# Kernel tuning notes

Measured on AMD Instinct MI355X. Metric: run time of the kernel, lower is better.

## Reference

```python
import jax, jax.numpy as jnp
import numpy as np

NUM_HEADS = 8


def _attn(q, k, v, scale):
    # q: [B,H,Nq,d], k/v: [B,H,Nk,d]
    a = jax.nn.softmax(jnp.einsum('bhqd,bhkd->bhqk', q, k) * scale, axis=-1)
    return jnp.einsum('bhqk,bhkd->bhqd', a, v)


def setup_inputs() -> dict:
    key = jax.random.key(0)
    k1, k2, k3 = jax.random.split(key, 3)
    B, N, C = 8, 1024, 768
    x = jax.random.normal(k1, (B, N, C), dtype=jnp.float32)
    w_qkv = jax.random.normal(k2, (3 * C, C), dtype=jnp.float32) * 0.02
    w_proj = jax.random.normal(k3, (C, C), dtype=jnp.float32) * 0.02
    b_proj = jnp.zeros((C,), dtype=jnp.float32)
    return {"x": x, "w_qkv": w_qkv, "w_proj": w_proj, "b_proj": b_proj}


def reference(x, w_qkv, w_proj, b_proj):
    B, N, C = x.shape
    H = NUM_HEADS
    hd = C // H            # full head dim (scale uses this, per the source)
    g = hd // 3            # per-group head dim
    scale = hd ** (-0.5)

    qkv = (x @ w_qkv.T).reshape(B, N, 3, H, hd).transpose(2, 0, 3, 1, 4)  # [3,B,H,N,hd]
    q, k, v = qkv[0], qkv[1], qkv[2]

    q3, q4, q5 = q[..., :g], q[..., g:2 * g], q[..., 2 * g:]
    k3, k4, k5 = k[..., :g], k[..., g:2 * g], k[..., 2 * g:]
    v3, v4, v5 = v[..., :g], v[..., g:2 * g], v[..., 2 * g:]

    def merge(o):  # [B,H,N,g] -> [B,N,H*g]
        return o.transpose(0, 2, 1, 3).reshape(B, N, C // 3)

    x3 = merge(_attn(q4, jnp.concatenate([k3, k4], axis=2), jnp.concatenate([v3, v4], axis=2), scale))
    x4 = merge(_attn(q5, jnp.concatenate([k3, k5], axis=2), jnp.concatenate([v3, v5], axis=2), scale))
    x5 = merge(_attn(q5, jnp.concatenate([k4, k5], axis=2), jnp.concatenate([v4, v5], axis=2), scale))

    out = jnp.concatenate([x3, x4, x5], axis=2)
    return out @ w_proj.T + b_proj
```

## Files before the change

kernel.cpp:

```cpp
#include <hip/hip_runtime.h>
#include <hip/hip_bf16.h>

typedef unsigned short u16;
typedef __attribute__((ext_vector_type(8))) short short8;
typedef __attribute__((ext_vector_type(4))) float f32x4;
typedef __attribute__((ext_vector_type(4))) unsigned uint32x4;

__device__ __forceinline__ u16 f2b(float f) {
  unsigned u = __builtin_bit_cast(unsigned, f);
  unsigned r = u + 0x7fffu + ((u >> 16) & 1u);
  return (u16)(r >> 16);
}

__device__ __forceinline__ unsigned pkbf16(float lo, float hi) {
  unsigned r;
  asm("v_cvt_pk_bf16_f32 %0, %1, %2" : "=v"(r) : "v"(lo), "v"(hi));
  return r;
}

#define GLD_LDS16(gp, lp) __builtin_amdgcn_global_load_lds( \
    (const __attribute__((address_space(1))) void*)(gp),    \
    (__attribute__((address_space(3))) void*)(lp), 16, 0, 0)

__global__ __launch_bounds__(256) void cvt3(
    const float* __restrict__ x, const float* __restrict__ wq, const float* __restrict__ wp,
    u16* __restrict__ xb, u16* __restrict__ wqb, u16* __restrict__ wpb)
{
  const int NX = 8192 * 768 / 4, NQ = 2304 * 768 / 4, NP = 768 * 768 / 4;
  int i = blockIdx.x * 256 + threadIdx.x;
  if (i < NX) {
    float4 v = *(const float4*)&x[(size_t)i * 4];
    uint2 pk; pk.x = pkbf16(v.x, v.y); pk.y = pkbf16(v.z, v.w);
    *(uint2*)&xb[(size_t)i * 4] = pk;
  } else if (i < NX + NQ) {
    int j = i - NX;
    float sc = (j < 147456) ? 0.14724447f : 1.0f;
    float4 v = *(const float4*)&wq[(size_t)j * 4];
    uint2 pk; pk.x = pkbf16(v.x * sc, v.y * sc); pk.y = pkbf16(v.z * sc, v.w * sc);
    *(uint2*)&wqb[(size_t)j * 4] = pk;
  } else if (i < NX + NQ + NP) {
    int j = i - NX - NQ;
    int oo = (j * 4) / 768, ii = (j * 4) % 768;
    int a = ii >> 8, h = (ii >> 5) & 7, c = ii & 31;
    float4 v = *(const float4*)&wp[(size_t)j * 4];
    uint2 pk; pk.x = pkbf16(v.x, v.y); pk.y = pkbf16(v.z, v.w);
    *(uint2*)&wpb[oo * 768 + h * 96 + a * 32 + c] = pk;
  }
}

__global__ __launch_bounds__(256) void gemm_bt(
    const u16* __restrict__ A, const u16* __restrict__ Bt,
    u16* __restrict__ Cb, float* __restrict__ Cf, const float* __restrict__ bias,
    u16* __restrict__ vt_out, int M, int N, int K)
{
  __shared__ u16 Al[128 * 32];
  __shared__ u16 Bl[128 * 32];
  const int tid = threadIdx.x;
  const int lane = tid & 63, wave = tid >> 6;
  const int wr = wave >> 1, wc = wave & 1;
  const int g = lane >> 4, c16 = lane & 15;
  const int m0 = blockIdx.y * 128, n0 = blockIdx.x * 128;

  f32x4 acc[4][4] = {};

  const int c0 = tid, c1 = tid + 256;
  const int r0 = c0 >> 2, o0 = (c0 & 3) * 8;
  const int r1 = c1 >> 2, o1 = (c1 & 3) * 8;
  const u16* a0 = A + (size_t)(m0 + r0) * K + o0;
  const u16* a1 = A + (size_t)(m0 + r1) * K + o1;
  const u16* b0 = Bt + (size_t)(n0 + r0) * K + o0;
  const u16* b1 = Bt + (size_t)(n0 + r1) * K + o1;

  for (int k0 = 0; k0 < K; k0 += 32) {
    GLD_LDS16(a0 + k0, Al + c0 * 8);
    GLD_LDS16(a1 + k0, Al + c1 * 8);
    GLD_LDS16(b0 + k0, Bl + c0 * 8);
    GLD_LDS16(b1 + k0, Bl + c1 * 8);
    __syncthreads();
    short8 af[4], bfr[4];
#pragma unroll
    for (int m = 0; m < 4; ++m)
      af[m] = *(const short8*)&Al[(wr * 64 + m * 16 + c16) * 32 + g * 8];
#pragma unroll
    for (int n = 0; n < 4; ++n)
      bfr[n] = *(const short8*)&Bl[(wc * 64 + n * 16 + c16) * 32 + g * 8];
#pragma unroll
    for (int m = 0; m < 4; ++m)
#pragma unroll
      for (int n = 0; n < 4; ++n)
        acc[m][n] = __builtin_amdgcn_mfma_f32_16x16x32_bf16(af[m], bfr[n], acc[m][n], 0, 0, 0);
    __syncthreads();
  }

  if (Cb) {
    if (vt_out && n0 >= 1536) {
#pragma unroll
      for (int m = 0; m < 4; ++m) {
        const int row0 = m0 + wr * 64 + m * 16 + g * 4;
        const int bb = row0 >> 10, nb = row0 & 1023;
        const int chunk = nb & ~31, o = nb & 31;
        const int slot0 = ((o >> 2) & 3) * 8 + ((o >> 4) & 1) * 4;
#pragma unroll
        for (int n = 0; n < 4; ++n) {
          const int colg = n0 - 1536 + wc * 64 + n * 16 + c16;
          const int hh = colg / 96, dd = colg % 96;
          uint2 pk;
          pk.x = pkbf16(acc[m][n][0], acc[m][n][1]);
          pk.y = pkbf16(acc[m][n][2], acc[m][n][3]);
          *(uint2*)&vt_out[((size_t)(bb * 8 + hh) * 96 + dd) * 1024 + chunk + slot0] = pk;
        }
      }
    } else {
#pragma unroll
      for (int m = 0; m < 4; ++m) {
        const int row = m0 + wr * 64 + m * 16 + g * 4;
#pragma unroll
        for (int n = 0; n < 4; ++n) {
          const int col = n0 + wc * 64 + n * 16 + c16;
#pragma unroll
          for (int j = 0; j < 4; ++j)
            Cb[(size_t)(row + j) * N + col] = f2b(acc[m][n][j]);
        }
      }
    }
  } else {
#pragma unroll
    for (int m = 0; m < 4; ++m) {
      const int row = m0 + wr * 64 + m * 16 + g * 4;
#pragma unroll
      for (int n = 0; n < 4; ++n) {
        const int col = n0 + wc * 64 + n * 16 + c16;
        const float bb = bias[col];
#pragma unroll
        for (int j = 0; j < 4; ++j)
          Cf[(size_t)(row + j) * N + col] = acc[m][n][j] + bb;
      }
    }
  }
}

__global__ __attribute__((amdgpu_flat_work_group_size(256, 256)))
__attribute__((amdgpu_waves_per_eu(2, 4)))
void attn_kernel(
    const u16* __restrict__ qkv, const u16* __restrict__ vt, u16* __restrict__ feat)
{
  __shared__ u16 smem[2 * 2560 + 64 * 72];
  u16* Kl = smem;
  u16* Vl = smem + 2 * 2560;

  const int tid = threadIdx.x;
  const int lane = tid & 63, wave = tid >> 6;
  const int g = lane >> 4, c16 = lane & 15;
  const int id = blockIdx.x;
  const int h = id & 7;
  const int r3 = id >> 3;
  const int aidx = r3 % 3;
  const int t2 = r3 / 3;
  const int qt = t2 & 7, b = t2 >> 3;
  const int bh = b * 8 + h;
  const int q0 = qt * 128 + wave * 32;
  const size_t tb = (size_t)b * 1024;

  const int p0 = (aidx == 2) ? 1 : 0;
  const int p1 = (aidx == 0) ? 1 : 2;
  const int qoff = (aidx == 0) ? 32 : 64;

  short8 qf[2];
#pragma unroll
  for (int m = 0; m < 2; ++m)
    qf[m] = *(const short8*)&qkv[(tb + q0 + m * 16 + c16) * 2304 + h * 96 + qoff + 8 * g];

  short8 ones;
#pragma unroll
  for (int i = 0; i < 8; ++i) ones[i] = (short)0x3F80;

  f32x4 acc[2][2] = {};
  f32x4 lsv[2] = {};

  const int kkey = tid >> 2, kcc = tid & 3;
  const int vd = tid >> 3, vc = tid & 7;
  const int P[2] = { p0, p1 };
  uint4 kst[2], vst[2];
#pragma unroll
  for (int i = 0; i < 2; ++i) {
    kst[i] = *(const uint4*)&qkv[(tb + kkey) * 2304 + 768 + h * 96 + P[i] * 32 + kcc * 8];
    vst[i] = *(const uint4*)&vt[((size_t)bh * 96 + P[i] * 32 + vd) * 1024 + vc * 8];
  }

  for (int t = 0; t < 16; ++t) {
    __syncthreads();
#pragma unroll
    for (int i = 0; i < 2; ++i) {
      *(uint4*)&Kl[i * 2560 + kkey * 40 + kcc * 8] = kst[i];
      *(uint4*)&Vl[(i * 32 + vd) * 72 + vc * 8] = vst[i];
    }
    if (t < 15) {
      int kv0 = (t + 1) * 64;
#pragma unroll
      for (int i = 0; i < 2; ++i) {
        kst[i] = *(const uint4*)&qkv[(tb + kv0 + kkey) * 2304 + 768 + h * 96 + P[i] * 32 + kcc * 8];
        vst[i] = *(const uint4*)&vt[((size_t)bh * 96 + P[i] * 32 + vd) * 1024 + kv0 + vc * 8];
      }
    }
    __syncthreads();

#pragma unroll
    for (int u = 0; u < 2; ++u) {
      short8 kf[4], vf[2][2];
#pragma unroll
      for (int n = 0; n < 4; ++n)
        kf[n] = *(const short8*)&Kl[u * 2560 + (n * 16 + c16) * 40 + g * 8];
#pragma unroll
      for (int n = 0; n < 2; ++n)
#pragma unroll
        for (int kk = 0; kk < 2; ++kk)
          vf[n][kk] = *(const short8*)&Vl[(u * 32 + n * 16 + c16) * 72 + kk * 32 + g * 8];

      const f32x4 z = {0.f, 0.f, 0.f, 0.f};
#pragma unroll
      for (int m = 0; m < 2; ++m) {
        f32x4 St[4];
        __builtin_amdgcn_s_setprio(1);
#pragma unroll
        for (int n = 0; n < 4; ++n)
          St[n] = __builtin_amdgcn_mfma_f32_16x16x32_bf16(kf[n], qf[m], z, 0, 0, 0);
        __builtin_amdgcn_s_setprio(0);
        short8 pa[2];
#pragma unroll
        for (int kk = 0; kk < 2; ++kk) {
          uint32x4 w;
          w.x = pkbf16(__builtin_amdgcn_exp2f(St[2 * kk][0]),     __builtin_amdgcn_exp2f(St[2 * kk][1]));
          w.y = pkbf16(__builtin_amdgcn_exp2f(St[2 * kk][2]),     __builtin_amdgcn_exp2f(St[2 * kk][3]));
          w.z = pkbf16(__builtin_amdgcn_exp2f(St[2 * kk + 1][0]), __builtin_amdgcn_exp2f(St[2 * kk + 1][1]));
          w.w = pkbf16(__builtin_amdgcn_exp2f(St[2 * kk + 1][2]), __builtin_amdgcn_exp2f(St[2 * kk + 1][3]));
          pa[kk] = __builtin_bit_cast(short8, w);
        }
        __builtin_amdgcn_s_setprio(1);
#pragma unroll
        for (int n = 0; n < 2; ++n)
#pragma unroll
          for (int kk = 0; kk < 2; ++kk)
            acc[m][n] = __builtin_amdgcn_mfma_f32_16x16x32_bf16(pa[kk], vf[n][kk], acc[m][n], 0, 0, 0);
#pragma unroll
        for (int kk = 0; kk < 2; ++kk)
          lsv[m] = __builtin_amdgcn_mfma_f32_16x16x32_bf16(pa[kk], ones, lsv[m], 0, 0, 0);
        __builtin_amdgcn_s_setprio(0);
      }
    }
  }

  __syncthreads();
  u16* Ol = smem + wave * 1024;
#pragma unroll
  for (int m = 0; m < 2; ++m) {
    f32x4 inv;
#pragma unroll
    for (int r = 0; r < 4; ++r) inv[r] = 1.0f / lsv[m][r];
#pragma unroll
    for (int n = 0; n < 2; ++n)
#pragma unroll
      for (int r = 0; r < 4; ++r)
        Ol[(m * 16 + g * 4 + r) * 32 + n * 16 + c16] = f2b(acc[m][n][r] * inv[r]);
  }
#pragma unroll
  for (int i = 0; i < 2; ++i) {
    int idx = lane + 64 * i;
    int row = idx >> 2, q4 = idx & 3;
    uint4 val = *(const uint4*)&Ol[row * 32 + q4 * 8];
    *(uint4*)&feat[(tb + q0 + row) * 768 + h * 96 + aidx * 32 + q4 * 8] = val;
  }
}

extern "C" void kernel_launch(void* const* d_in, const int* in_sizes, int n_in,
                              void* d_out, int out_size, void* d_ws, size_t ws_size,
                              hipStream_t stream) {
  const float* x  = (const float*)d_in[0];
  const float* wq = (const float*)d_in[1];
  const float* wp = (const float*)d_in[2];
  const float* bp = (const float*)d_in[3];
  float* out = (float*)d_out;

  char* ws = (char*)d_ws;
  u16* xb    = (u16*)(ws);
  u16* wqb   = (u16*)(ws + 12582912);
  u16* wpb   = (u16*)(ws + 16121856);
  u16* qkvb  = (u16*)(ws + 17301504);
  u16* vtb   = (u16*)(ws + 55050240);
  u16* featb = xb;

  cvt3<<<8448, 256, 0, stream>>>(x, wq, wp, xb, wqb, wpb);
  gemm_bt<<<dim3(18, 64), 256, 0, stream>>>(xb, wqb, qkvb, nullptr, nullptr, vtb, 8192, 2304, 768);
  attn_kernel<<<1536, 256, 0, stream>>>(qkvb, vtb, featb);
  gemm_bt<<<dim3(6, 64), 256, 0, stream>>>(featb, wpb, nullptr, out, bp, nullptr, 8192, 768, 768);
}
```

Before: 172.7 us.

## Add 128x64 projection GEMM, double-buffer and swizzle attention K/V LDS

The output projection now runs on a new 128x64-tile GEMM kernel, doubling the block count from 384 to 768 so more CUs have work on the small N=768 problem. The attention kernel double-buffers its K/V shared-memory tiles, which removes one __syncthreads per iteration. It also replaces the padded row strides with XOR-swizzled layouts to avoid LDS bank conflicts without padding. The cost is more shared memory per attention block, which may lower occupancy, and smaller tiles with less reuse in the projection GEMM.

Measured after the change: 197.0 us. +14.1%, slower.

```diff
diff --git a/kernel.cpp b/kernel.cpp
--- a/kernel.cpp
+++ b/kernel.cpp
@@ -50,8 +50,7 @@
 
 __global__ __launch_bounds__(256) void gemm_bt(
     const u16* __restrict__ A, const u16* __restrict__ Bt,
-    u16* __restrict__ Cb, float* __restrict__ Cf, const float* __restrict__ bias,
-    u16* __restrict__ vt_out, int M, int N, int K)
+    u16* __restrict__ Cb, u16* __restrict__ vt_out, int M, int N, int K)
 {
   __shared__ u16 Al[128 * 32];
   __shared__ u16 Bl[128 * 32];
@@ -92,35 +91,21 @@
     __syncthreads();
   }
 
-  if (Cb) {
-    if (vt_out && n0 >= 1536) {
-#pragma unroll
-      for (int m = 0; m < 4; ++m) {
-        const int row0 = m0 + wr * 64 + m * 16 + g * 4;
-        const int bb = row0 >> 10, nb = row0 & 1023;
-        const int chunk = nb & ~31, o = nb & 31;
-        const int slot0 = ((o >> 2) & 3) * 8 + ((o >> 4) & 1) * 4;
-#pragma unroll
-        for (int n = 0; n < 4; ++n) {
-          const int colg = n0 - 1536 + wc * 64 + n * 16 + c16;
-          const int hh = colg / 96, dd = colg % 96;
-          uint2 pk;
-          pk.x = pkbf16(acc[m][n][0], acc[m][n][1]);
-          pk.y = pkbf16(acc[m][n][2], acc[m][n][3]);
-          *(uint2*)&vt_out[((size_t)(bb * 8 + hh) * 96 + dd) * 1024 + chunk + slot0] = pk;
-        }
-      }
-    } else {
-#pragma unroll
-      for (int m = 0; m < 4; ++m) {
-        const int row = m0 + wr * 64 + m * 16 + g * 4;
-#pragma unroll
-        for (int n = 0; n < 4; ++n) {
-          const int col = n0 + wc * 64 + n * 16 + c16;
-#pragma unroll
-          for (int j = 0; j < 4; ++j)
-            Cb[(size_t)(row + j) * N + col] = f2b(acc[m][n][j]);
-        }
+  if (vt_out && n0 >= 1536) {
+#pragma unroll
+    for (int m = 0; m < 4; ++m) {
+      const int row0 = m0 + wr * 64 + m * 16 + g * 4;
+      const int bb = row0 >> 10, nb = row0 & 1023;
+      const int chunk = nb & ~31, o = nb & 31;
+      const int slot0 = ((o >> 2) & 3) * 8 + ((o >> 4) & 1) * 4;
+#pragma unroll
+      for (int n = 0; n < 4; ++n) {
+        const int colg = n0 - 1536 + wc * 64 + n * 16 + c16;
+        const int hh = colg / 96, dd = colg % 96;
+        uint2 pk;
+        pk.x = pkbf16(acc[m][n][0], acc[m][n][1]);
+        pk.y = pkbf16(acc[m][n][2], acc[m][n][3]);
+        *(uint2*)&vt_out[((size_t)(bb * 8 + hh) * 96 + dd) * 1024 + chunk + slot0] = pk;
       }
     }
   } else {
@@ -130,11 +115,64 @@
 #pragma unroll
       for (int n = 0; n < 4; ++n) {
         const int col = n0 + wc * 64 + n * 16 + c16;
-        const float bb = bias[col];
 #pragma unroll
         for (int j = 0; j < 4; ++j)
-          Cf[(size_t)(row + j) * N + col] = acc[m][n][j] + bb;
-      }
+          Cb[(size_t)(row + j) * N + col] = f2b(acc[m][n][j]);
+      }
+    }
+  }
+}
+
+__global__ __launch_bounds__(256) void gemm_bt64(
+    const u16* __restrict__ A, const u16* __restrict__ Bt,
+    float* __restrict__ Cf, const float* __restrict__ bias, int M, int N, int K)
+{
+  __shared__ u16 Al[128 * 32];
+  __shared__ u16 Bl[64 * 32];
+  const int tid = threadIdx.x;
+  const int lane = tid & 63, wave = tid >> 6;
+  const int g = lane >> 4, c16 = lane & 15;
+  const int m0 = blockIdx.y * 128, n0 = blockIdx.x * 64;
+
+  f32x4 acc[2][4] = {};
+
+  const int c0 = tid, c1 = tid + 256;
+  const int rA0 = c0 >> 2, oA0 = (c0 & 3) * 8;
+  const int rA1 = c1 >> 2, oA1 = (c1 & 3) * 8;
+  const u16* a0 = A + (size_t)(m0 + rA0) * K + oA0;
+  const u16* a1 = A + (size_t)(m0 + rA1) * K + oA1;
+  const u16* b0 = Bt + (size_t)(n0 + rA0) * K + oA0;
+
+  for (int k0 = 0; k0 < K; k0 += 32) {
+    GLD_LDS16(a0 + k0, Al + c0 * 8);
+    GLD_LDS16(a1 + k0, Al + c1 * 8);
+    if (tid < 256) GLD_LDS16(b0 + k0, Bl + c0 * 8);
+    __syncthreads();
+    short8 af[2], bfr[4];
+#pragma unroll
+    for (int m = 0; m < 2; ++m)
+      af[m] = *(const short8*)&Al[(wave * 32 + m * 16 + c16) * 32 + g * 8];
+#pragma unroll
+    for (int n = 0; n < 4; ++n)
+      bfr[n] = *(const short8*)&Bl[(n * 16 + c16) * 32 + g * 8];
+#pragma unroll
+    for (int m = 0; m < 2; ++m)
+#pragma unroll
+      for (int n = 0; n < 4; ++n)
+        acc[m][n] = __builtin_amdgcn_mfma_f32_16x16x32_bf16(af[m], bfr[n], acc[m][n], 0, 0, 0);
+    __syncthreads();
+  }
+
+#pragma unroll
+  for (int m = 0; m < 2; ++m) {
+    const int row = m0 + wave * 32 + m * 16 + g * 4;
+#pragma unroll
+    for (int n = 0; n < 4; ++n) {
+      const int col = n0 + n * 16 + c16;
+      const float bb = bias[col];
+#pragma unroll
+      for (int j = 0; j < 4; ++j)
+        Cf[(size_t)(row + j) * N + col] = acc[m][n][j] + bb;
     }
   }
 }
@@ -144,9 +182,7 @@
 void attn_kernel(
     const u16* __restrict__ qkv, const u16* __restrict__ vt, u16* __restrict__ feat)
 {
-  __shared__ u16 smem[2 * 2560 + 64 * 72];
-  u16* Kl = smem;
-  u16* Vl = smem + 2 * 2560;
+  __shared__ u16 smem[20480];
 
   const int tid = threadIdx.x;
   const int lane = tid & 63, wave = tid >> 6;
@@ -186,13 +222,16 @@
     kst[i] = *(const uint4*)&qkv[(tb + kkey) * 2304 + 768 + h * 96 + P[i] * 32 + kcc * 8];
     vst[i] = *(const uint4*)&vt[((size_t)bh * 96 + P[i] * 32 + vd) * 1024 + vc * 8];
   }
+  const int kwr = kkey * 32 + (kcc ^ (kkey & 3)) * 8;
+  const int vwr = vd * 64 + (vc ^ (vd & 7)) * 8;
 
   for (int t = 0; t < 16; ++t) {
-    __syncthreads();
+    u16* Kb = smem + (t & 1) * 8192;
+    u16* Vb = Kb + 4096;
 #pragma unroll
     for (int i = 0; i < 2; ++i) {
-      *(uint4*)&Kl[i * 2560 + kkey * 40 + kcc * 8] = kst[i];
-      *(uint4*)&Vl[(i * 32 + vd) * 72 + vc * 8] = vst[i];
+      *(uint4*)&Kb[i * 2048 + kwr] = kst[i];
+      *(uint4*)&Vb[i * 2048 + vwr] = vst[i];
     }
     if (t < 15) {
       int kv0 = (t + 1) * 64;
@@ -208,13 +247,17 @@
     for (int u = 0; u < 2; ++u) {
       short8 kf[4], vf[2][2];
 #pragma unroll
-      for (int n = 0; n < 4; ++n)
-        kf[n] = *(const short8*)&Kl[u * 2560 + (n * 16 + c16) * 40 + g * 8];
+      for (int n = 0; n < 4; ++n) {
+        const int row = n * 16 + c16;
+        kf[n] = *(const short8*)&Kb[u * 2048 + row * 32 + ((g ^ (c16 & 3)) * 8)];
+      }
 #pragma unroll
       for (int n = 0; n < 2; ++n)
 #pragma unroll
-        for (int kk = 0; kk < 2; ++kk)
-          vf[n][kk] = *(const short8*)&Vl[(u * 32 + n * 16 + c16) * 72 + kk * 32 + g * 8];
+        for (int kk = 0; kk < 2; ++kk) {
+          const int row = n * 16 + c16;
+          vf[n][kk] = *(const short8*)&Vb[u * 2048 + row * 64 + (((kk * 4 + g) ^ (c16 & 7)) * 8)];
+        }
 
       const f32x4 z = {0.f, 0.f, 0.f, 0.f};
 #pragma unroll
@@ -249,8 +292,7 @@
     }
   }
 
-  __syncthreads();
-  u16* Ol = smem + wave * 1024;
+  u16* Ol = smem + 16384 + wave * 1024;
 #pragma unroll
   for (int m = 0; m < 2; ++m) {
     f32x4 inv;
@@ -289,7 +331,7 @@
   u16* featb = xb;
 
   cvt3<<<8448, 256, 0, stream>>>(x, wq, wp, xb, wqb, wpb);
-  gemm_bt<<<dim3(18, 64), 256, 0, stream>>>(xb, wqb, qkvb, nullptr, nullptr, vtb, 8192, 2304, 768);
+  gemm_bt<<<dim3(18, 64), 256, 0, stream>>>(xb, wqb, qkvb, vtb, 8192, 2304, 768);
   attn_kernel<<<1536, 256, 0, stream>>>(qkvb, vtb, featb);
-  gemm_bt<<<dim3(6, 64), 256, 0, stream>>>(featb, wpb, nullptr, out, bp, nullptr, 8192, 768, 768);
-}
+  gemm_bt64<<<dim3(12, 64), 256, 0, stream>>>(featb, wpb, out, bp, 8192, 768, 768);
+}
```
